# Optimization experiments

Measured on AMD Instinct MI355X. Metric: run time of the kernel, lower is better.

The kernel has to match this reference:

```python
import jax, jax.numpy as jnp
import numpy as np

EMBED_DIM = 1024
NUM_HEADS = 16
HEAD_DIM = EMBED_DIM // NUM_HEADS
BATCH = 2
SEQ = 2048


def setup_inputs() -> dict:
    key = jax.random.key(0)
    k1, k2, k3, k4, k5 = jax.random.split(key, 5)
    scale_in = 1.0 / np.sqrt(EMBED_DIM)
    return {
        "x": jax.random.normal(k1, (BATCH, SEQ, EMBED_DIM), dtype=jnp.float32),
        "head_mask": jnp.ones((NUM_HEADS,), dtype=jnp.float32),
        "qkv_w": jax.random.normal(k2, (3 * EMBED_DIM, EMBED_DIM), dtype=jnp.float32) * scale_in,
        "qkv_b": jax.random.normal(k3, (3 * EMBED_DIM,), dtype=jnp.float32) * 0.02,
        "fc_w": jax.random.normal(k4, (EMBED_DIM, EMBED_DIM), dtype=jnp.float32) * scale_in,
        "fc_b": jax.random.normal(k5, (EMBED_DIM,), dtype=jnp.float32) * 0.02,
    }


def reference(x, head_mask, qkv_w, qkv_b, fc_w, fc_b):
    N, S, D = x.shape
    H, hd = NUM_HEADS, HEAD_DIM
    # qkv Linear: y = x @ W^T + b -> [N, S, 3D]
    qkv = jnp.einsum("nsd,ed->nse", x, qkv_w) + qkv_b
    # reshape (N, S, H, 3, hd) then permute(3,0,2,1,4) -> (3, N, H, S, hd)
    qkv = qkv.reshape(N, S, H, 3, hd).transpose(3, 0, 2, 1, 4)
    q, k, v = qkv[0], qkv[1], qkv[2]
    hm = head_mask.reshape(1, H, 1, 1)
    q = q * hm
    k = k * hm
    v = v * hm
    # scores [N, H, S, S]
    energy = jnp.einsum("nhqd,nhkd->nhqk", q, k)
    attention = jax.nn.softmax(energy / jnp.sqrt(jnp.float32(hd)), axis=-1)
    out = jnp.einsum("nhqk,nhkd->nhqd", attention, v)
    out = out.transpose(0, 2, 1, 3).reshape(N, S, H * hd)
    out = jnp.einsum("nsd,ed->nse", out, fc_w) + fc_b
    return out
```

## Files before the change

kernel.cpp:

```cpp
#include <hip/hip_runtime.h>
#include <hip/hip_bf16.h>

typedef __bf16 bf16;
typedef __attribute__((ext_vector_type(8))) __bf16 bf16x8;
typedef __attribute__((ext_vector_type(4))) __bf16 bf16x4;
typedef __attribute__((ext_vector_type(4))) float f32x4;
typedef __attribute__((ext_vector_type(4))) unsigned int uint4x;

#if __has_builtin(__builtin_amdgcn_exp2f)
#define EXP2F(x) __builtin_amdgcn_exp2f(x)
#else
#define EXP2F(x) exp2f(x)
#endif

#define AS1 __attribute__((address_space(1)))
#define AS3 __attribute__((address_space(3)))

static __device__ __forceinline__ void async_ld16(const bf16* g, bf16* l) {
  __builtin_amdgcn_global_load_lds((const AS1 void*)g, (AS3 void*)l, 16, 0, 0);
}

static __device__ __forceinline__ unsigned bf16rne(float x) {
  unsigned u = __float_as_uint(x);
  return (u + 0x7fffu + ((u >> 16) & 1u)) >> 16;
}
static __device__ __forceinline__ unsigned pack2(float a, float b) {
  return bf16rne(a) | (bf16rne(b) << 16);
}

__global__ void cvt3_kernel(const float* __restrict__ x, const float* __restrict__ qw,
                            const float* __restrict__ fw, bf16* __restrict__ xb,
                            bf16* __restrict__ qwb, bf16* __restrict__ fwb) {
  int b = blockIdx.x;
  const float* src;
  bf16* dst;
  int i;
  if (b < 4096) { src = x; dst = xb; i = b * 256 + threadIdx.x; }
  else if (b < 7168) { src = qw; dst = qwb; i = (b - 4096) * 256 + threadIdx.x; }
  else { src = fw; dst = fwb; i = (b - 7168) * 256 + threadIdx.x; }
  f32x4 v = *(const f32x4*)(src + (size_t)i * 4);
  bf16x4 o;
  o[0] = (bf16)v[0]; o[1] = (bf16)v[1]; o[2] = (bf16)v[2]; o[3] = (bf16)v[3];
  *(bf16x4*)(dst + (size_t)i * 4) = o;
}

template <int MODE>
__global__ __launch_bounds__(256, 2) void gemm_bt_kernel(
    const bf16* __restrict__ A, const bf16* __restrict__ Bw,
    const float* __restrict__ bias, const float* __restrict__ hm,
    bf16* __restrict__ Qp, bf16* __restrict__ Kp, bf16* __restrict__ Vp,
    float* __restrict__ outF, int Ncols, int Kdim, int rowBlkCount) {
  __shared__ bf16 As[128 * 32];
  __shared__ bf16 Bs[128 * 32];
  const int t = threadIdx.x, lane = t & 63, w = t >> 6;
  const int wr = w >> 1, wc = w & 1;
  const int j = lane & 15, quad = lane >> 4;
  const int rowBlk = blockIdx.x % rowBlkCount;
  const int colBlk = blockIdx.x / rowBlkCount;
  const int rowBase = rowBlk * 128, colBase = colBlk * 128;

  f32x4 acc[4][4];
  const f32x4 z4 = {0.f, 0.f, 0.f, 0.f};
#pragma unroll
  for (int i = 0; i < 4; ++i)
#pragma unroll
    for (int jj = 0; jj < 4; ++jj) acc[i][jj] = z4;

  const int f0 = t * 8;
  const int f1 = f0 + 2048;
  const int r0 = f0 >> 5, c0 = f0 & 31;
  const int r1 = f1 >> 5, c1 = f1 & 31;

  for (int k0 = 0; k0 < Kdim; k0 += 32) {
    async_ld16(A + (size_t)(rowBase + r0) * Kdim + k0 + c0, &As[f0]);
    async_ld16(A + (size_t)(rowBase + r1) * Kdim + k0 + c1, &As[f1]);
    async_ld16(Bw + (size_t)(colBase + r0) * Kdim + k0 + c0, &Bs[f0]);
    async_ld16(Bw + (size_t)(colBase + r1) * Kdim + k0 + c1, &Bs[f1]);
    __syncthreads();
    bf16x8 af[4], bfr[4];
#pragma unroll
    for (int i = 0; i < 4; ++i)
      af[i] = *(const bf16x8*)&As[(wr * 64 + i * 16 + j) * 32 + quad * 8];
#pragma unroll
    for (int jj = 0; jj < 4; ++jj)
      bfr[jj] = *(const bf16x8*)&Bs[(wc * 64 + jj * 16 + j) * 32 + quad * 8];
#pragma unroll
    for (int i = 0; i < 4; ++i)
#pragma unroll
      for (int jj = 0; jj < 4; ++jj)
        acc[i][jj] = __builtin_amdgcn_mfma_f32_16x16x32_bf16(af[i], bfr[jj], acc[i][jj], 0, 0, 0);
    __syncthreads();
  }

  if (MODE == 0) {
#pragma unroll
    for (int jj = 0; jj < 4; ++jj) {
      int col = colBase + wc * 64 + jj * 16 + j;
      int hh = col / 192;
      int rem = col - hh * 192;
      int mm = rem >> 6;
      int dd = rem & 63;
      float hmv = hm[hh];
      float bv = bias[col];
      float sc = (mm == 0) ? hmv * 0.18033688011112042f : hmv;
#pragma unroll
      for (int i = 0; i < 4; ++i) {
#pragma unroll
        for (int r = 0; r < 4; ++r) {
          int row = rowBase + wr * 64 + i * 16 + quad * 4 + r;
          int n = row >> 11, ss = row & 2047;
          size_t nh = (size_t)(n * 16 + hh);
          float val = (acc[i][jj][r] + bv) * sc;
          if (mm == 0) {
            Qp[nh * 131072 + ss * 64 + dd] = (bf16)val;
          } else if (mm == 1) {
            size_t idx = nh * 131072 + (size_t)(ss >> 7) * 8192 +
                         (size_t)(2 * ((ss >> 5) & 3) + ((ss >> 2) & 1)) * 1024 +
                         (dd >> 5) * 512 + ((dd >> 3) & 3) * 128 +
                         (((ss >> 3) & 3) * 4 + (ss & 3)) * 8 + (dd & 7);
            Kp[idx] = (bf16)val;
          } else {
            size_t idx = nh * 131072 + (size_t)(ss >> 7) * 8192 +
                         (((ss >> 5) & 3) * 4 + (dd >> 4)) * 512 +
                         ((ss >> 3) & 3) * 128 + (dd & 15) * 8 + (ss & 7);
            Vp[idx] = (bf16)val;
          }
        }
      }
    }
  } else {
#pragma unroll
    for (int jj = 0; jj < 4; ++jj) {
      int col = colBase + wc * 64 + jj * 16 + j;
      float bv = bias[col];
#pragma unroll
      for (int i = 0; i < 4; ++i)
#pragma unroll
        for (int r = 0; r < 4; ++r) {
          int row = rowBase + wr * 64 + i * 16 + quad * 4 + r;
          outF[(size_t)row * Ncols + col] = acc[i][jj][r] + bv;
        }
    }
  }
}

__global__ __launch_bounds__(256, 4) void flash_kernel(const bf16* __restrict__ Qp,
                                                       const bf16* __restrict__ Kf,
                                                       const bf16* __restrict__ Vf,
                                                       float* __restrict__ O0,
                                                       float* __restrict__ O1,
                                                       float* __restrict__ Lp) {
  __shared__ bf16 Ks[8192];
  __shared__ bf16 Vs[8192];
  const int t = threadIdx.x, lane = t & 63, w = t >> 6;
  const int j = lane & 15, quad = lane >> 4;
  const int g = blockIdx.x & 63;
  const int qt = blockIdx.x >> 6;
  const int nh = g >> 1, ck = g & 1;
  const int q0 = qt * 128 + w * 32;
  const bf16* Qb = Qp + (size_t)nh * 131072;
  const bf16* Kc = Kf + (size_t)nh * 131072 + ck * 65536;
  const bf16* Vc = Vf + (size_t)nh * 131072 + ck * 65536;

  bf16x8 qf[2][2];
#pragma unroll
  for (int rt = 0; rt < 2; ++rt)
#pragma unroll
    for (int kd = 0; kd < 2; ++kd)
      qf[rt][kd] = *(const bf16x8*)&Qb[(size_t)(q0 + rt * 16 + j) * 64 + kd * 32 + quad * 8];

  float lrow[2] = {0.f, 0.f};
  f32x4 oacc[2][4];
  const f32x4 z4 = {0.f, 0.f, 0.f, 0.f};
#pragma unroll
  for (int rt = 0; rt < 2; ++rt)
#pragma unroll
    for (int dt = 0; dt < 4; ++dt) oacc[rt][dt] = z4;

#pragma unroll
  for (int p = 0; p < 4; ++p) {
    int c = (p * 256 + t) * 8;
    async_ld16(Kc + c, &Ks[c]);
    async_ld16(Vc + c, &Vs[c]);
  }

  for (int it = 0; it < 8; ++it) {
    __syncthreads();

    unsigned pkd[2][8][2];
#pragma unroll
    for (int ct = 0; ct < 8; ++ct) {
      bf16x8 kf0 = *(const bf16x8*)&Ks[ct * 1024 + lane * 8];
      bf16x8 kf1 = *(const bf16x8*)&Ks[ct * 1024 + 512 + lane * 8];
#pragma unroll
      for (int rt = 0; rt < 2; ++rt) {
        f32x4 sv = z4;
        sv = __builtin_amdgcn_mfma_f32_16x16x32_bf16(kf0, qf[rt][0], sv, 0, 0, 0);
        sv = __builtin_amdgcn_mfma_f32_16x16x32_bf16(kf1, qf[rt][1], sv, 0, 0, 0);
        float p0 = EXP2F(sv[0]), p1 = EXP2F(sv[1]);
        float p2 = EXP2F(sv[2]), p3 = EXP2F(sv[3]);
        lrow[rt] += (p0 + p1) + (p2 + p3);
        pkd[rt][ct][0] = pack2(p0, p1);
        pkd[rt][ct][1] = pack2(p2, p3);
      }
    }

#pragma unroll
    for (int kk = 0; kk < 4; ++kk) {
      union { uint4x u; bf16x8 h; } pa[2];
#pragma unroll
      for (int rt = 0; rt < 2; ++rt)
        pa[rt].u = (uint4x){pkd[rt][2 * kk][0], pkd[rt][2 * kk][1],
                            pkd[rt][2 * kk + 1][0], pkd[rt][2 * kk + 1][1]};
#pragma unroll
      for (int dt = 0; dt < 4; ++dt) {
        bf16x8 vf = *(const bf16x8*)&Vs[(kk * 4 + dt) * 512 + lane * 8];
        oacc[0][dt] = __builtin_amdgcn_mfma_f32_16x16x32_bf16(pa[0].h, vf, oacc[0][dt], 0, 0, 0);
        oacc[1][dt] = __builtin_amdgcn_mfma_f32_16x16x32_bf16(pa[1].h, vf, oacc[1][dt], 0, 0, 0);
      }
    }

    __syncthreads();
    if (it < 7) {
      const bf16* kn = Kc + (it + 1) * 8192;
      const bf16* vn = Vc + (it + 1) * 8192;
#pragma unroll
      for (int p = 0; p < 4; ++p) {
        int c = (p * 256 + t) * 8;
        async_ld16(kn + c, &Ks[c]);
        async_ld16(vn + c, &Vs[c]);
      }
    }
  }

  float* Od = ck ? O1 : O0;
#pragma unroll
  for (int rt = 0; rt < 2; ++rt) {
    float l = lrow[rt];
    l += __shfl_xor(l, 16);
    l += __shfl_xor(l, 32);
    if (quad == 0) Lp[ck * 65536 + (size_t)nh * 2048 + q0 + rt * 16 + j] = l;
#pragma unroll
    for (int r = 0; r < 4; ++r) {
      int srow = q0 + rt * 16 + quad * 4 + r;
      size_t row = (size_t)nh * 2048 + srow;
#pragma unroll
      for (int dt = 0; dt < 4; ++dt)
        Od[row * 64 + dt * 16 + j] = oacc[rt][dt][r];
    }
  }
}

__global__ __launch_bounds__(256) void merge_kernel(const float* __restrict__ O0,
                                                    const float* __restrict__ O1,
                                                    const float* __restrict__ Lp,
                                                    bf16* __restrict__ attn) {
  int g = blockIdx.x * 256 + threadIdx.x;
  int row = g >> 4;
  int dg = (g & 15) * 4;
  float inv = 1.0f / (Lp[row] + Lp[65536 + row]);
  f32x4 a = *(const f32x4*)(O0 + (size_t)row * 64 + dg);
  f32x4 b = *(const f32x4*)(O1 + (size_t)row * 64 + dg);
  int nh = row >> 11, s = row & 2047;
  int n = nh >> 4, h = nh & 15;
  bf16x4 o;
#pragma unroll
  for (int i = 0; i < 4; ++i) o[i] = (bf16)((a[i] + b[i]) * inv);
  *(bf16x4*)(attn + ((size_t)(n * 2048 + s)) * 1024 + h * 64 + dg) = o;
}

extern "C" void kernel_launch(void* const* d_in, const int* in_sizes, int n_in,
                              void* d_out, int out_size, void* d_ws, size_t ws_size,
                              hipStream_t stream) {
  const float* x = (const float*)d_in[0];
  const float* head_mask = (const float*)d_in[1];
  const float* qkv_w = (const float*)d_in[2];
  const float* qkv_b = (const float*)d_in[3];
  const float* fc_w = (const float*)d_in[4];
  const float* fc_b = (const float*)d_in[5];
  float* out = (float*)d_out;

  char* ws = (char*)d_ws;
  bf16* x_bf    = (bf16*)(ws + 0);
  bf16* qkvw_bf = (bf16*)(ws + ((size_t)8 << 20));
  bf16* fcw_bf  = (bf16*)(ws + ((size_t)14 << 20));
  bf16* Qp      = (bf16*)(ws + ((size_t)16 << 20));
  bf16* Kf      = (bf16*)(ws + ((size_t)24 << 20));
  bf16* Vf      = (bf16*)(ws + ((size_t)32 << 20));
  float* O1     = (float*)(ws + ((size_t)40 << 20));
  float* Lp     = (float*)(ws + ((size_t)56 << 20));
  float* O0     = (float*)d_out;
  bf16* attn = x_bf;

  cvt3_kernel<<<8192, 256, 0, stream>>>(x, qkv_w, fc_w, x_bf, qkvw_bf, fcw_bf);
  gemm_bt_kernel<0><<<32 * 24, 256, 0, stream>>>(x_bf, qkvw_bf, qkv_b, head_mask,
                                                 Qp, Kf, Vf, nullptr, 3072, 1024, 32);
  flash_kernel<<<1024, 256, 0, stream>>>(Qp, Kf, Vf, O0, O1, Lp);
  merge_kernel<<<4096, 256, 0, stream>>>(O0, O1, Lp, attn);
  gemm_bt_kernel<1><<<32 * 8, 256, 0, stream>>>(attn, fcw_bf, fc_b, nullptr,
                                                nullptr, nullptr, nullptr, out, 1024, 1024, 32);
}
```

Measured before the change: 219.1 us.

## Double-buffer K/V tiles in flash attention to overlap loads with compute

Splits the K/V shared-memory tile into two half-size ping-pong buffers. The next half-tile's async global-to-LDS load is issued before computing on the current buffer, so memory latency can overlap with the MFMA and exp work. Total LDS and barrier count stay the same. The overlap may be limited if the compiler waits on all outstanding loads at each barrier, and the smaller tiles give less unrolled work per step.

```diff
diff --git a/kernel.cpp b/kernel.cpp
--- a/kernel.cpp
+++ b/kernel.cpp
@@ -144,14 +144,63 @@
   }
 }
 
+#define FLASH_STAGE(tileIdx, KsBuf, VsBuf)                                  \
+  {                                                                         \
+    const bf16* kn_ = Kc + (tileIdx) * 4096;                                \
+    const bf16* vn_ = Vc + (tileIdx) * 4096;                                \
+    _Pragma("unroll")                                                       \
+    for (int p = 0; p < 2; ++p) {                                           \
+      int c = (p * 256 + t) * 8;                                            \
+      async_ld16(kn_ + c, &KsBuf[c]);                                       \
+      async_ld16(vn_ + c, &VsBuf[c]);                                       \
+    }                                                                       \
+  }
+
+#define FLASH_TILE(KsBuf, VsBuf)                                            \
+  {                                                                         \
+    unsigned pkd[2][4][2];                                                  \
+    _Pragma("unroll")                                                       \
+    for (int ct = 0; ct < 4; ++ct) {                                        \
+      bf16x8 kf0 = *(const bf16x8*)&KsBuf[ct * 1024 + lane * 8];            \
+      bf16x8 kf1 = *(const bf16x8*)&KsBuf[ct * 1024 + 512 + lane * 8];      \
+      _Pragma("unroll")                                                     \
+      for (int rt = 0; rt < 2; ++rt) {                                      \
+        f32x4 sv = z4;                                                      \
+        sv = __builtin_amdgcn_mfma_f32_16x16x32_bf16(kf0, qf[rt][0], sv, 0, 0, 0); \
+        sv = __builtin_amdgcn_mfma_f32_16x16x32_bf16(kf1, qf[rt][1], sv, 0, 0, 0); \
+        float p0 = EXP2F(sv[0]), p1 = EXP2F(sv[1]);                         \
+        float p2 = EXP2F(sv[2]), p3 = EXP2F(sv[3]);                         \
+        lrow[rt] += (p0 + p1) + (p2 + p3);                                  \
+        pkd[rt][ct][0] = pack2(p0, p1);                                     \
+        pkd[rt][ct][1] = pack2(p2, p3);                                     \
+      }                                                                     \
+    }                                                                       \
+    _Pragma("unroll")                                                       \
+    for (int kk = 0; kk < 2; ++kk) {                                        \
+      union { uint4x u; bf16x8 h; } pa[2];                                  \
+      _Pragma("unroll")                                                     \
+      for (int rt = 0; rt < 2; ++rt)                                        \
+        pa[rt].u = (uint4x){pkd[rt][2 * kk][0], pkd[rt][2 * kk][1],         \
+                            pkd[rt][2 * kk + 1][0], pkd[rt][2 * kk + 1][1]};\
+      _Pragma("unroll")                                                     \
+      for (int dt = 0; dt < 4; ++dt) {                                      \
+        bf16x8 vf = *(const bf16x8*)&VsBuf[(kk * 4 + dt) * 512 + lane * 8]; \
+        oacc[0][dt] = __builtin_amdgcn_mfma_f32_16x16x32_bf16(pa[0].h, vf, oacc[0][dt], 0, 0, 0); \
+        oacc[1][dt] = __builtin_amdgcn_mfma_f32_16x16x32_bf16(pa[1].h, vf, oacc[1][dt], 0, 0, 0); \
+      }                                                                     \
+    }                                                                       \
+  }
+
 __global__ __launch_bounds__(256, 4) void flash_kernel(const bf16* __restrict__ Qp,
                                                        const bf16* __restrict__ Kf,
                                                        const bf16* __restrict__ Vf,
                                                        float* __restrict__ O0,
                                                        float* __restrict__ O1,
                                                        float* __restrict__ Lp) {
-  __shared__ bf16 Ks[8192];
-  __shared__ bf16 Vs[8192];
+  __shared__ bf16 Ks0[4096];
+  __shared__ bf16 Vs0[4096];
+  __shared__ bf16 Ks1[4096];
+  __shared__ bf16 Vs1[4096];
   const int t = threadIdx.x, lane = t & 63, w = t >> 6;
   const int j = lane & 15, quad = lane >> 4;
   const int g = blockIdx.x & 63;
@@ -177,60 +226,15 @@
 #pragma unroll
     for (int dt = 0; dt < 4; ++dt) oacc[rt][dt] = z4;
 
-#pragma unroll
-  for (int p = 0; p < 4; ++p) {
-    int c = (p * 256 + t) * 8;
-    async_ld16(Kc + c, &Ks[c]);
-    async_ld16(Vc + c, &Vs[c]);
-  }
-
-  for (int it = 0; it < 8; ++it) {
+  FLASH_STAGE(0, Ks0, Vs0);
+
+  for (int it2 = 0; it2 < 8; ++it2) {
     __syncthreads();
-
-    unsigned pkd[2][8][2];
-#pragma unroll
-    for (int ct = 0; ct < 8; ++ct) {
-      bf16x8 kf0 = *(const bf16x8*)&Ks[ct * 1024 + lane * 8];
-      bf16x8 kf1 = *(const bf16x8*)&Ks[ct * 1024 + 512 + lane * 8];
-#pragma unroll
-      for (int rt = 0; rt < 2; ++rt) {
-        f32x4 sv = z4;
-        sv = __builtin_amdgcn_mfma_f32_16x16x32_bf16(kf0, qf[rt][0], sv, 0, 0, 0);
-        sv = __builtin_amdgcn_mfma_f32_16x16x32_bf16(kf1, qf[rt][1], sv, 0, 0, 0);
-        float p0 = EXP2F(sv[0]), p1 = EXP2F(sv[1]);
-        float p2 = EXP2F(sv[2]), p3 = EXP2F(sv[3]);
-        lrow[rt] += (p0 + p1) + (p2 + p3);
-        pkd[rt][ct][0] = pack2(p0, p1);
-        pkd[rt][ct][1] = pack2(p2, p3);
-      }
-    }
-
-#pragma unroll
-    for (int kk = 0; kk < 4; ++kk) {
-      union { uint4x u; bf16x8 h; } pa[2];
-#pragma unroll
-      for (int rt = 0; rt < 2; ++rt)
-        pa[rt].u = (uint4x){pkd[rt][2 * kk][0], pkd[rt][2 * kk][1],
-                            pkd[rt][2 * kk + 1][0], pkd[rt][2 * kk + 1][1]};
-#pragma unroll
-      for (int dt = 0; dt < 4; ++dt) {
-        bf16x8 vf = *(const bf16x8*)&Vs[(kk * 4 + dt) * 512 + lane * 8];
-        oacc[0][dt] = __builtin_amdgcn_mfma_f32_16x16x32_bf16(pa[0].h, vf, oacc[0][dt], 0, 0, 0);
-        oacc[1][dt] = __builtin_amdgcn_mfma_f32_16x16x32_bf16(pa[1].h, vf, oacc[1][dt], 0, 0, 0);
-      }
-    }
-
+    FLASH_STAGE(it2 * 2 + 1, Ks1, Vs1);
+    FLASH_TILE(Ks0, Vs0);
     __syncthreads();
-    if (it < 7) {
-      const bf16* kn = Kc + (it + 1) * 8192;
-      const bf16* vn = Vc + (it + 1) * 8192;
-#pragma unroll
-      for (int p = 0; p < 4; ++p) {
-        int c = (p * 256 + t) * 8;
-        async_ld16(kn + c, &Ks[c]);
-        async_ld16(vn + c, &Vs[c]);
-      }
-    }
+    if (it2 < 7) FLASH_STAGE(it2 * 2 + 2, Ks0, Vs0);
+    FLASH_TILE(Ks1, Vs1);
   }
 
   float* Od = ck ? O1 : O0;
```

Measured after the change: 205.9 us. 6.0% less time.
